# Optimization experiments

Measured on AMD Instinct MI355X. Metric: run time of the kernel, lower is better.

Reference implementation:

```python
import jax, jax.numpy as jnp
import numpy as np

HIDDEN = 2048
NUM_HEADS = 16
Q_LORA = 1536
KV_LORA = 512
QK_NOPE = 128
QK_ROPE = 64
V_HEAD = 128
EPS = 1e-6
QK_HEAD = QK_NOPE + QK_ROPE  # 192


def rmsnorm(x, w, eps=EPS):
    xf = x.astype(jnp.float32)
    var = jnp.mean(xf * xf, axis=-1, keepdims=True)
    return (w * (xf * jax.lax.rsqrt(var + eps)).astype(x.dtype))


def setup_inputs() -> dict:
    key = jax.random.key(0)
    ks = jax.random.split(key, 8)
    B, S = 1, 2048
    hidden_states = jax.random.normal(ks[0], (B, S, HIDDEN), dtype=jnp.float32)
    # causal additive mask [B,1,S,S]
    causal = jnp.tril(jnp.ones((S, S), dtype=bool))
    attention_mask = jnp.where(causal, 0.0, -1e9).astype(jnp.float32)[None, None]
    s = lambda fan_in: 1.0 / np.sqrt(fan_in)
    Wqa = jax.random.normal(ks[1], (HIDDEN, Q_LORA), dtype=jnp.float32) * s(HIDDEN)
    gqa = jnp.ones((Q_LORA,), dtype=jnp.float32)
    Wqb = jax.random.normal(ks[2], (Q_LORA, NUM_HEADS * QK_HEAD), dtype=jnp.float32) * s(Q_LORA)
    Wkva = jax.random.normal(ks[3], (HIDDEN, KV_LORA + QK_ROPE), dtype=jnp.float32) * s(HIDDEN)
    gkva = jnp.ones((KV_LORA,), dtype=jnp.float32)
    Wkvb = jax.random.normal(ks[4], (KV_LORA, NUM_HEADS * (QK_NOPE + V_HEAD)), dtype=jnp.float32) * s(KV_LORA)
    Wo = jax.random.normal(ks[5], (NUM_HEADS * V_HEAD, HIDDEN), dtype=jnp.float32) * s(NUM_HEADS * V_HEAD)
    return {"hidden_states": hidden_states, "attention_mask": attention_mask,
            "Wqa": Wqa, "gqa": gqa, "Wqb": Wqb, "Wkva": Wkva, "gkva": gkva,
            "Wkvb": Wkvb, "Wo": Wo}


def reference(hidden_states, attention_mask, Wqa, gqa, Wqb, Wkva, gkva, Wkvb, Wo):
    B, S, _ = hidden_states.shape
    # Q path: low-rank down-proj + RMSNorm + up-proj
    q_c = rmsnorm(hidden_states @ Wqa, gqa)
    q = (q_c @ Wqb).reshape(B, S, NUM_HEADS, QK_HEAD).transpose(0, 2, 1, 3)  # [B,H,S,192]
    # KV path: joint down-proj, split latent and shared rope part
    kv_c = hidden_states @ Wkva  # [B,S,KV_LORA+ROPE]
    kv_a, k_rope = kv_c[..., :KV_LORA], kv_c[..., KV_LORA:]
    kv = (rmsnorm(kv_a, gkva) @ Wkvb).reshape(B, S, NUM_HEADS, QK_NOPE + V_HEAD)
    k_nope, v = kv[..., :QK_NOPE], kv[..., QK_NOPE:]
    # shared rope part broadcast across heads (no rotary actually applied in source)
    k_rope_b = jnp.broadcast_to(k_rope[:, :, None, :], (B, S, NUM_HEADS, QK_ROPE))
    k = jnp.concatenate([k_nope, k_rope_b], axis=-1).transpose(0, 2, 1, 3)  # [B,H,S,192]
    v = v.transpose(0, 2, 1, 3)  # [B,H,S,128]
    scale = 1.0 / np.sqrt(QK_HEAD)
    attn = jnp.einsum("bhqd,bhkd->bhqk", q, k) * scale
    attn = attn + attention_mask
    attn = jax.nn.softmax(attn.astype(jnp.float32), axis=-1).astype(v.dtype)
    out = jnp.einsum("bhqk,bhkd->bhqd", attn, v)  # [B,H,S,128]
    out = out.transpose(0, 2, 1, 3).reshape(B, S, NUM_HEADS * V_HEAD)
    return out @ Wo
```

## Files before the change

### kernel.cpp

```cpp
#include <hip/hip_runtime.h>
#include <hip/hip_bf16.h>

typedef __bf16 bf16;
typedef __bf16 bf16x8 __attribute__((ext_vector_type(8)));
typedef __bf16 bf16x4 __attribute__((ext_vector_type(4)));
typedef float f32x4 __attribute__((ext_vector_type(4)));

#define HIDDEN 2048
#define SEQ 2048
#define NH 16
#define QL 1536
#define KVL 512
#define SCALE_LOG2E 0.10411754631f

__device__ __forceinline__ void gload_lds16(const void* g, void* l) {
  typedef const __attribute__((address_space(1))) void* gp_t;
  typedef __attribute__((address_space(3))) void* lp_t;
  __builtin_amdgcn_global_load_lds((gp_t)(unsigned long long)g,
                                   (lp_t)(unsigned int)(unsigned long long)l, 16, 0, 0);
}

__device__ __forceinline__ float fexp2(float x) {
  float r; asm("v_exp_f32 %0, %1" : "=v"(r) : "v"(x)); return r;
}

__global__ void k_prep(const float* __restrict__ hidden, bf16* __restrict__ Xb,
                       const float* __restrict__ Wqa, bf16* __restrict__ WqaT,
                       const float* __restrict__ Wqb, bf16* __restrict__ WqbT,
                       const float* __restrict__ Wkva, bf16* __restrict__ WkvaT,
                       const float* __restrict__ Wkvb, bf16* __restrict__ WkvbT,
                       const float* __restrict__ Wo, bf16* __restrict__ WoT) {
  __shared__ float tile[32][33];
  int b = blockIdx.x, tid = threadIdx.x;
  const float* W; bf16* Wt; int K, N, bx, by;
  if (b < 3072)       { W = Wqa;  Wt = WqaT;  K = 2048; N = 1536; int r = b;         bx = r % 48;  by = r / 48; }
  else if (b < 7680)  { W = Wqb;  Wt = WqbT;  K = 1536; N = 3072; int r = b - 3072;  bx = r % 96;  by = r / 96; }
  else if (b < 8832)  { W = Wkva; Wt = WkvaT; K = 2048; N = 576;  int r = b - 7680;  bx = r % 18;  by = r / 18; }
  else if (b < 10880) { W = Wkvb; Wt = WkvbT; K = 512;  N = 4096; int r = b - 8832;  bx = r % 128; by = r / 128; }
  else if (b < 14976) { W = Wo;   Wt = WoT;   K = 2048; N = 2048; int r = b - 10880; bx = r % 64;  by = r / 64; }
  else {
    int r = b - 14976;
    int base = (r * 256 + tid) * 4;
    float4 v = *(const float4*)(hidden + base);
    bf16x4 o = { (bf16)v.x, (bf16)v.y, (bf16)v.z, (bf16)v.w };
    *(bf16x4*)(Xb + base) = o;
    return;
  }
  int n0 = bx * 32, k0 = by * 32, cc = tid & 31, rr = tid >> 5;
#pragma unroll
  for (int it = 0; it < 4; ++it) {
    int r = it * 8 + rr;
    tile[r][cc] = W[(size_t)(k0 + r) * N + n0 + cc];
  }
  __syncthreads();
#pragma unroll
  for (int it = 0; it < 4; ++it) {
    int r = it * 8 + rr;
    Wt[(size_t)(n0 + r) * K + k0 + cc] = (bf16)tile[cc][r];
  }
}

__device__ __forceinline__ void gemm_body(const bf16* __restrict__ A, const bf16* __restrict__ Bt,
                                          bf16* __restrict__ Cb, float* __restrict__ Cf,
                                          int N, int K, int m0, int n0, bf16* As, bf16* Bs) {
  int tid = threadIdx.x, lane = tid & 63, w = tid >> 6;
  int wr = w >> 1, wc = w & 1;
  int l15 = lane & 15, l4 = lane >> 4;
  f32x4 acc[4][4] = {};
  for (int k0 = 0; k0 < K; k0 += 64) {
#pragma unroll
    for (int i = 0; i < 4; ++i) {
      int c = w * 4 + i;
      int row = c * 8 + (lane >> 3);
      int col = (lane & 7) * 8;
      gload_lds16(&A[(size_t)(m0 + row) * K + k0 + col], &As[c * 512]);
      gload_lds16(&Bt[(size_t)(n0 + row) * K + k0 + col], &Bs[c * 512]);
    }
    __syncthreads();
#pragma unroll
    for (int kk = 0; kk < 2; ++kk) {
      bf16x8 af[4], bfr[4];
#pragma unroll
      for (int m = 0; m < 4; ++m)
        af[m] = *(const bf16x8*)&As[(wr * 64 + m * 16 + l15) * 64 + kk * 32 + l4 * 8];
#pragma unroll
      for (int n = 0; n < 4; ++n)
        bfr[n] = *(const bf16x8*)&Bs[(wc * 64 + n * 16 + l15) * 64 + kk * 32 + l4 * 8];
      __builtin_amdgcn_s_setprio(1);
#pragma unroll
      for (int m = 0; m < 4; ++m)
#pragma unroll
        for (int n = 0; n < 4; ++n)
          acc[m][n] = __builtin_amdgcn_mfma_f32_16x16x32_bf16(af[m], bfr[n], acc[m][n], 0, 0, 0);
      __builtin_amdgcn_s_setprio(0);
    }
    __syncthreads();
  }
#pragma unroll
  for (int m = 0; m < 4; ++m)
#pragma unroll
    for (int n = 0; n < 4; ++n)
#pragma unroll
      for (int r = 0; r < 4; ++r) {
        int grow = m0 + wr * 64 + m * 16 + l4 * 4 + r;
        int gcol = n0 + wc * 64 + n * 16 + l15;
        if (gcol < N) {
          float v = acc[m][n][r];
          if (Cf) Cf[(size_t)grow * N + gcol] = v;
          else Cb[(size_t)grow * N + gcol] = (bf16)v;
        }
      }
}

__global__ __launch_bounds__(256) void k_gemm(const bf16* __restrict__ A, const bf16* __restrict__ Bt,
                                              bf16* __restrict__ Cb, float* __restrict__ Cf,
                                              int N, int K) {
  __shared__ __align__(16) bf16 As[128 * 64];
  __shared__ __align__(16) bf16 Bs[128 * 64];
  gemm_body(A, Bt, Cb, Cf, N, K, blockIdx.x * 128, blockIdx.y * 128, As, Bs);
}

__global__ __launch_bounds__(256) void k_gemm_a(const bf16* __restrict__ Xb,
                                                const bf16* __restrict__ B1, const bf16* __restrict__ B2,
                                                float* __restrict__ C1, float* __restrict__ C2) {
  __shared__ __align__(16) bf16 As[128 * 64];
  __shared__ __align__(16) bf16 Bs[128 * 64];
  int by = blockIdx.y;
  if (by < 12) gemm_body(Xb, B1, nullptr, C1, 1536, 2048, blockIdx.x * 128, by * 128, As, Bs);
  else         gemm_body(Xb, B2, nullptr, C2, 576, 2048, blockIdx.x * 128, (by - 12) * 128, As, Bs);
}

__global__ __launch_bounds__(256) void k_gemm_b(const bf16* __restrict__ A1, const bf16* __restrict__ A2,
                                                const bf16* __restrict__ B1, const bf16* __restrict__ B2,
                                                bf16* __restrict__ C1, bf16* __restrict__ C2) {
  __shared__ __align__(16) bf16 As[128 * 64];
  __shared__ __align__(16) bf16 Bs[128 * 64];
  int by = blockIdx.y;
  if (by < 24) gemm_body(A1, B1, C1, nullptr, 3072, 1536, blockIdx.x * 128, by * 128, As, Bs);
  else         gemm_body(A2, B2, C2, nullptr, 4096, 512, blockIdx.x * 128, (by - 24) * 128, As, Bs);
}

__device__ inline float block_reduce_sum(float v, float* red) {
#pragma unroll
  for (int off = 1; off < 64; off <<= 1) v += __shfl_xor(v, off);
  int w = threadIdx.x >> 6;
  if ((threadIdx.x & 63) == 0) red[w] = v;
  __syncthreads();
  return red[0] + red[1] + red[2] + red[3];
}

__global__ void k_rms_all(const float* __restrict__ qa, const float* __restrict__ gq, bf16* __restrict__ qc,
                          const float* __restrict__ kvc, const float* __restrict__ gkv,
                          bf16* __restrict__ kvn, bf16* __restrict__ kr) {
  __shared__ float red[4];
  int b = blockIdx.x, tid = threadIdx.x;
  if (b < 2048) {
    int row = b;
    float v[6];
    float ss = 0.f;
#pragma unroll
    for (int j = 0; j < 6; ++j) {
      v[j] = qa[(size_t)row * QL + tid + j * 256];
      ss += v[j] * v[j];
    }
    float tot = block_reduce_sum(ss, red);
    float rs = rsqrtf(tot / (float)QL + 1e-6f);
#pragma unroll
    for (int j = 0; j < 6; ++j) {
      int c = tid + j * 256;
      qc[(size_t)row * QL + c] = (bf16)(v[j] * rs * gq[c]);
    }
  } else {
    int row = b - 2048;
    float v0 = kvc[(size_t)row * 576 + tid];
    float v1 = kvc[(size_t)row * 576 + tid + 256];
    float tot = block_reduce_sum(v0 * v0 + v1 * v1, red);
    float rs = rsqrtf(tot / (float)KVL + 1e-6f);
    kvn[(size_t)row * KVL + tid] = (bf16)(v0 * rs * gkv[tid]);
    kvn[(size_t)row * KVL + tid + 256] = (bf16)(v1 * rs * gkv[tid + 256]);
    if (tid < 64) kr[row * 64 + tid] = (bf16)kvc[(size_t)row * 576 + 512 + tid];
  }
}

__global__ void k_vt(const bf16* __restrict__ KVm, bf16* __restrict__ VT) {
  __shared__ bf16 tile[32][34];
  int b = blockIdx.x, tid = threadIdx.x;
  int h = b >> 8, rem = b & 255;
  int d0 = (rem >> 6) * 32, s0 = (rem & 63) * 32;
  int cc = tid & 31, rr = tid >> 5;
#pragma unroll
  for (int it = 0; it < 4; ++it) {
    int r = it * 8 + rr;
    tile[r][cc] = KVm[(size_t)(s0 + r) * 4096 + h * 256 + 128 + d0 + cc];
  }
  __syncthreads();
#pragma unroll
  for (int it = 0; it < 4; ++it) {
    int r = it * 8 + rr;
    VT[((size_t)(h * 128 + d0 + r)) * 2048 + s0 + cc] = tile[cc][r];
  }
}

__global__ __launch_bounds__(256) void k_attn(const bf16* __restrict__ Q, const bf16* __restrict__ KV,
                                              const bf16* __restrict__ KR, const bf16* __restrict__ VT,
                                              bf16* __restrict__ O) {
  __shared__ __align__(16) bf16 Ks[64 * 200];
  __shared__ __align__(16) bf16 Vt[128 * 72];
  __shared__ __align__(16) bf16 Ps[4 * 16 * 72];
  int bid = blockIdx.x;
  int h = bid & 15, i = bid >> 4;
  int qb = (i < 16) ? i : 47 - i;
  int q0 = qb * 64;
  int tid = threadIdx.x, lane = tid & 63, w = tid >> 6;
  int l15 = lane & 15, l4 = lane >> 4;
  bf16* Pw = Ps + w * 16 * 72;
  const bf16* VTh = VT + (size_t)h * 128 * 2048;

  bf16x8 aq[6];
  int qrow = q0 + w * 16 + l15;
#pragma unroll
  for (int ks = 0; ks < 6; ++ks)
    aq[ks] = *(const bf16x8*)&Q[(size_t)qrow * 3072 + h * 192 + ks * 32 + l4 * 8];

  bf16x8 ones_b;
  {
    float ov = (l15 == 0) ? 1.0f : 0.0f;
#pragma unroll
    for (int j = 0; j < 8; ++j) ones_b[j] = (bf16)ov;
  }

  f32x4 oacc[8] = {};
  f32x4 o9 = {0.f, 0.f, 0.f, 0.f};
  float m[4] = {-1e30f, -1e30f, -1e30f, -1e30f};
  int nt = qb + 1;
  for (int t = 0; t < nt; ++t) {
#pragma unroll
    for (int it = 0; it < 6; ++it) {
      int idx = it * 256 + tid;
      int r = idx / 24, gg = idx % 24;
      int p = t * 64 + r;
      int4 val;
      if (gg < 16) val = *(const int4*)&KV[(size_t)p * 4096 + h * 256 + gg * 8];
      else         val = *(const int4*)&KR[(size_t)p * 64 + (gg - 16) * 8];
      *(int4*)&Ks[r * 200 + gg * 8] = val;
    }
#pragma unroll
    for (int it = 0; it < 4; ++it) {
      int idx = it * 256 + tid;
      int d = idx >> 3, c = idx & 7;
      *(int4*)&Vt[d * 72 + c * 8] = *(const int4*)&VTh[(size_t)d * 2048 + t * 64 + c * 8];
    }
    __syncthreads();

    f32x4 sacc[4] = {};
    __builtin_amdgcn_s_setprio(1);
#pragma unroll
    for (int ks = 0; ks < 6; ++ks)
#pragma unroll
      for (int n = 0; n < 4; ++n) {
        bf16x8 bk = *(const bf16x8*)&Ks[(n * 16 + l15) * 200 + ks * 32 + l4 * 8];
        sacc[n] = __builtin_amdgcn_mfma_f32_16x16x32_bf16(aq[ks], bk, sacc[n], 0, 0, 0);
      }
    __builtin_amdgcn_s_setprio(0);

    bool lastt = (t == nt - 1);
#pragma unroll
    for (int n = 0; n < 4; ++n)
#pragma unroll
      for (int r = 0; r < 4; ++r) {
        float v = sacc[n][r] * SCALE_LOG2E;
        if (lastt) {
          int col = t * 64 + n * 16 + l15;
          int rowg = q0 + w * 16 + l4 * 4 + r;
          if (col > rowg) v = -1e30f;
        }
        sacc[n][r] = v;
      }

    float pmax[4];
#pragma unroll
    for (int r = 0; r < 4; ++r) {
      float mx = fmaxf(fmaxf(sacc[0][r], sacc[1][r]), fmaxf(sacc[2][r], sacc[3][r]));
      mx = fmaxf(mx, __shfl_xor(mx, 1));
      mx = fmaxf(mx, __shfl_xor(mx, 2));
      mx = fmaxf(mx, __shfl_xor(mx, 4));
      mx = fmaxf(mx, __shfl_xor(mx, 8));
      pmax[r] = mx;
    }
    float need = 0.f;
#pragma unroll
    for (int r = 0; r < 4; ++r) need = fmaxf(need, pmax[r] - m[r]);
    if (__any(need > 8.0f)) {
#pragma unroll
      for (int r = 0; r < 4; ++r) {
        float mn = fmaxf(m[r], pmax[r]);
        float al = fexp2(m[r] - mn);
        m[r] = mn;
#pragma unroll
        for (int vf = 0; vf < 8; ++vf) oacc[vf][r] *= al;
        o9[r] *= al;
      }
    }

#pragma unroll
    for (int n = 0; n < 4; ++n)
#pragma unroll
      for (int r = 0; r < 4; ++r)
        Pw[(l4 * 4 + r) * 72 + n * 16 + l15] = (bf16)fexp2(sacc[n][r] - m[r]);

    __builtin_amdgcn_s_setprio(1);
#pragma unroll
    for (int ks = 0; ks < 2; ++ks) {
      bf16x8 ap = *(const bf16x8*)&Pw[l15 * 72 + ks * 32 + l4 * 8];
      o9 = __builtin_amdgcn_mfma_f32_16x16x32_bf16(ap, ones_b, o9, 0, 0, 0);
#pragma unroll
      for (int vf = 0; vf < 8; ++vf) {
        bf16x8 bv = *(const bf16x8*)&Vt[(vf * 16 + l15) * 72 + ks * 32 + l4 * 8];
        oacc[vf] = __builtin_amdgcn_mfma_f32_16x16x32_bf16(ap, bv, oacc[vf], 0, 0, 0);
      }
    }
    __builtin_amdgcn_s_setprio(0);
    __syncthreads();
  }

#pragma unroll
  for (int r = 0; r < 4; ++r) {
    float ls = __shfl(o9[r], lane & 48);
    float inv = 1.0f / ls;
#pragma unroll
    for (int vf = 0; vf < 8; ++vf) {
      int rowg = q0 + w * 16 + l4 * 4 + r;
      int col = h * 128 + vf * 16 + l15;
      O[(size_t)rowg * 2048 + col] = (bf16)(oacc[vf][r] * inv);
    }
  }
}

extern "C" void kernel_launch(void* const* d_in, const int* in_sizes, int n_in,
                              void* d_out, int out_size, void* d_ws, size_t ws_size,
                              hipStream_t stream) {
  (void)in_sizes; (void)n_in; (void)out_size; (void)ws_size;
  const float* hidden = (const float*)d_in[0];
  const float* Wqa  = (const float*)d_in[2];
  const float* gqa  = (const float*)d_in[3];
  const float* Wqb  = (const float*)d_in[4];
  const float* Wkva = (const float*)d_in[5];
  const float* gkva = (const float*)d_in[6];
  const float* Wkvb = (const float*)d_in[7];
  const float* Wo   = (const float*)d_in[8];
  float* out = (float*)d_out;

  char* ws = (char*)d_ws;
  size_t off = 0;
  auto alloc = [&](size_t bytes) {
    char* p = ws + off;
    off += (bytes + 255) & ~(size_t)255;
    return p;
  };
  bf16* Xb     = (bf16*)alloc((size_t)SEQ * HIDDEN * 2);
  bf16* WqaT   = (bf16*)alloc((size_t)QL * HIDDEN * 2);
  bf16* WqbT   = (bf16*)alloc((size_t)3072 * QL * 2);
  bf16* WkvaT  = (bf16*)alloc((size_t)576 * HIDDEN * 2);
  bf16* WkvbT  = (bf16*)alloc((size_t)4096 * KVL * 2);
  bf16* WoT    = (bf16*)alloc((size_t)2048 * 2048 * 2);
  float* qa    = (float*)alloc((size_t)SEQ * QL * 4);
  float* kvc   = (float*)alloc((size_t)SEQ * 576 * 4);
  bf16* qc     = (bf16*)alloc((size_t)SEQ * QL * 2);
  bf16* kvn    = (bf16*)alloc((size_t)SEQ * KVL * 2);
  bf16* krope  = (bf16*)alloc((size_t)SEQ * 64 * 2);
  bf16* Qm     = (bf16*)alloc((size_t)SEQ * 3072 * 2);
  bf16* KVm    = (bf16*)alloc((size_t)SEQ * 4096 * 2);
  bf16* VTg    = (bf16*)alloc((size_t)NH * 128 * SEQ * 2);
  bf16* Om     = (bf16*)alloc((size_t)SEQ * 2048 * 2);

  k_prep<<<19072, 256, 0, stream>>>(hidden, Xb, Wqa, WqaT, Wqb, WqbT,
                                    Wkva, WkvaT, Wkvb, WkvbT, Wo, WoT);
  k_gemm_a<<<dim3(16, 17), 256, 0, stream>>>(Xb, WqaT, WkvaT, qa, kvc);
  k_rms_all<<<4096, 256, 0, stream>>>(qa, gqa, qc, kvc, gkva, kvn, krope);
  k_gemm_b<<<dim3(16, 56), 256, 0, stream>>>(qc, kvn, WqbT, WkvbT, Qm, KVm);
  k_vt<<<4096, 256, 0, stream>>>(KVm, VTg);
  k_attn<<<512, 256, 0, stream>>>(Qm, KVm, krope, VTg, Om);
  k_gemm<<<dim3(16, 16), 256, 0, stream>>>(Om, WoT, nullptr, out, 2048, 2048);
}
```

Baseline: 244.6 us.

## Split causal attention KV range into chunks with separate combine kernel

Splits each query block's KV loop into chunks of up to 8 tiles (flash-decoding style), raising the grid from 512 to 1280 blocks. Blocks covering more than one chunk write unnormalized bf16 partial outputs plus (max, sum) pairs, and a new combine kernel merges them with log-sum-exp weights. The aim is better load balance and CU occupancy for the long causal rows. The cost is an extra launch, extra partial-output traffic, and bf16 rounding of the unnormalized partials. Partial outputs reuse the qa scratch buffer, which is dead by then.

```diff
diff --git a/kernel.cpp b/kernel.cpp
--- a/kernel.cpp
+++ b/kernel.cpp
@@ -203,13 +203,20 @@
 
 __global__ __launch_bounds__(256) void k_attn(const bf16* __restrict__ Q, const bf16* __restrict__ KV,
                                               const bf16* __restrict__ KR, const bf16* __restrict__ VT,
-                                              bf16* __restrict__ O) {
+                                              bf16* __restrict__ O,
+                                              bf16* __restrict__ Opart, float2* __restrict__ Ml) {
   __shared__ __align__(16) bf16 Ks[64 * 200];
   __shared__ __align__(16) bf16 Vt[128 * 72];
   __shared__ __align__(16) bf16 Ps[4 * 16 * 72];
   int bid = blockIdx.x;
-  int h = bid & 15, i = bid >> 4;
-  int qb = (i < 16) ? i : 47 - i;
+  int h = bid & 15, cid = bid >> 4;
+  int qb, ch, nc;
+  if (cid < 8)       { qb = cid; ch = 0; nc = 1; }
+  else if (cid < 24) { int r = cid - 8;  qb = 8 + (r >> 1); ch = r & 1; nc = 2; }
+  else if (cid < 48) { int r = cid - 24; qb = 16 + r / 3;   ch = r % 3; nc = 3; }
+  else               { int r = cid - 48; qb = 24 + (r >> 2); ch = r & 3; nc = 4; }
+  int t0 = ch * 8;
+  int t1 = t0 + 8 < qb + 1 ? t0 + 8 : qb + 1;
   int q0 = qb * 64;
   int tid = threadIdx.x, lane = tid & 63, w = tid >> 6;
   int l15 = lane & 15, l4 = lane >> 4;
@@ -232,8 +239,7 @@
   f32x4 oacc[8] = {};
   f32x4 o9 = {0.f, 0.f, 0.f, 0.f};
   float m[4] = {-1e30f, -1e30f, -1e30f, -1e30f};
-  int nt = qb + 1;
-  for (int t = 0; t < nt; ++t) {
+  for (int t = t0; t < t1; ++t) {
 #pragma unroll
     for (int it = 0; it < 6; ++it) {
       int idx = it * 256 + tid;
@@ -263,7 +269,7 @@
       }
     __builtin_amdgcn_s_setprio(0);
 
-    bool lastt = (t == nt - 1);
+    bool lastt = (t == qb);
 #pragma unroll
     for (int n = 0; n < 4; ++n)
 #pragma unroll
@@ -323,16 +329,62 @@
     __syncthreads();
   }
 
-#pragma unroll
-  for (int r = 0; r < 4; ++r) {
-    float ls = __shfl(o9[r], lane & 48);
-    float inv = 1.0f / ls;
-#pragma unroll
-    for (int vf = 0; vf < 8; ++vf) {
-      int rowg = q0 + w * 16 + l4 * 4 + r;
-      int col = h * 128 + vf * 16 + l15;
-      O[(size_t)rowg * 2048 + col] = (bf16)(oacc[vf][r] * inv);
-    }
+  if (nc == 1) {
+#pragma unroll
+    for (int r = 0; r < 4; ++r) {
+      float ls = __shfl(o9[r], lane & 48);
+      float inv = 1.0f / ls;
+#pragma unroll
+      for (int vf = 0; vf < 8; ++vf) {
+        int rowg = q0 + w * 16 + l4 * 4 + r;
+        int col = h * 128 + vf * 16 + l15;
+        O[(size_t)rowg * 2048 + col] = (bf16)(oacc[vf][r] * inv);
+      }
+    }
+  } else {
+    bf16* Op = Opart + (size_t)bid * 64 * 128;
+#pragma unroll
+    for (int r = 0; r < 4; ++r) {
+      int row = w * 16 + l4 * 4 + r;
+#pragma unroll
+      for (int vf = 0; vf < 8; ++vf)
+        Op[row * 128 + vf * 16 + l15] = (bf16)oacc[vf][r];
+      if (l15 == 0) Ml[bid * 64 + row] = make_float2(m[r], o9[r]);
+    }
+  }
+}
+
+__global__ __launch_bounds__(256) void k_comb(const bf16* __restrict__ Opart,
+                                              const float2* __restrict__ Ml,
+                                              bf16* __restrict__ O) {
+  int b = blockIdx.x, h = b & 15, qb = 8 + (b >> 4);
+  int cid0, nc;
+  if (qb < 16)      { cid0 = 8 + 2 * (qb - 8);   nc = 2; }
+  else if (qb < 24) { cid0 = 24 + 3 * (qb - 16); nc = 3; }
+  else              { cid0 = 48 + 4 * (qb - 24); nc = 4; }
+  int tid = threadIdx.x;
+  int rr = tid >> 5, col = (tid & 31) * 4;
+  int slot0 = cid0 * 16 + h;
+#pragma unroll
+  for (int rp = 0; rp < 8; ++rp) {
+    int row = rp * 8 + rr;
+    float M = -1e30f;
+    for (int c = 0; c < nc; ++c) M = fmaxf(M, Ml[(slot0 + c * 16) * 64 + row].x);
+    float acc0 = 0.f, acc1 = 0.f, acc2 = 0.f, acc3 = 0.f, L = 0.f;
+    for (int c = 0; c < nc; ++c) {
+      int slot = slot0 + c * 16;
+      float2 ml = Ml[slot * 64 + row];
+      float wgt = fexp2(ml.x - M);
+      L += wgt * ml.y;
+      bf16x4 v = *(const bf16x4*)&Opart[(size_t)slot * 64 * 128 + row * 128 + col];
+      acc0 += wgt * (float)v[0];
+      acc1 += wgt * (float)v[1];
+      acc2 += wgt * (float)v[2];
+      acc3 += wgt * (float)v[3];
+    }
+    float inv = 1.0f / L;
+    bf16x4 o = { (bf16)(acc0 * inv), (bf16)(acc1 * inv), (bf16)(acc2 * inv), (bf16)(acc3 * inv) };
+    *(bf16x4*)&O[(size_t)(qb * 64 + row) * 2048 + h * 128 + col] = o;
   }
 }
 
@@ -372,6 +424,8 @@
   bf16* KVm    = (bf16*)alloc((size_t)SEQ * 4096 * 2);
   bf16* VTg    = (bf16*)alloc((size_t)NH * 128 * SEQ * 2);
   bf16* Om     = (bf16*)alloc((size_t)SEQ * 2048 * 2);
+  float2* Ml   = (float2*)alloc((size_t)1280 * 64 * 8);
+  bf16* Opart  = (bf16*)qa;
 
   k_prep<<<19072, 256, 0, stream>>>(hidden, Xb, Wqa, WqaT, Wqb, WqbT,
                                     Wkva, WkvaT, Wkvb, WkvbT, Wo, WoT);
@@ -379,6 +433,7 @@
   k_rms_all<<<4096, 256, 0, stream>>>(qa, gqa, qc, kvc, gkva, kvn, krope);
   k_gemm_b<<<dim3(16, 56), 256, 0, stream>>>(qc, kvn, WqbT, WkvbT, Qm, KVm);
   k_vt<<<4096, 256, 0, stream>>>(KVm, VTg);
-  k_attn<<<512, 256, 0, stream>>>(Qm, KVm, krope, VTg, Om);
+  k_attn<<<1280, 256, 0, stream>>>(Qm, KVm, krope, VTg, Om, Opart, Ml);
+  k_comb<<<384, 256, 0, stream>>>(Opart, Ml, Om);
   k_gemm<<<dim3(16, 16), 256, 0, stream>>>(Om, WoT, nullptr, out, 2048, 2048);
 }
```

Result: slower. 252.8 us (+3.3%).

## Swizzle attention LDS tiles, use direct global-to-LDS loads and transposed MFMA

Applied to the files above, without the earlier changes.

Rewrites the attention kernel's inner loop. K and V tiles are now loaded with global_load_lds into XOR-swizzled, unpadded LDS layouts instead of going through registers into padded arrays. The MFMA operands are swapped so each lane holds one query column, which lets the row max and row sum be computed with two cross-lane shuffles and a scalar running state. That removes the extra ones-vector MFMA used for the row sum. P is packed with v_cvt_pk_bf16, and the output goes through a swizzled LDS transpose so it can be written with 16-byte stores. The aim is fewer VGPR round-trips, less shuffle and sum overhead, and better-coalesced writes, at the cost of more complex swizzle address arithmetic.

```diff
diff --git a/kernel.cpp b/kernel.cpp
--- a/kernel.cpp
+++ b/kernel.cpp
@@ -22,6 +22,9 @@
 
 __device__ __forceinline__ float fexp2(float x) {
   float r; asm("v_exp_f32 %0, %1" : "=v"(r) : "v"(x)); return r;
+}
+__device__ __forceinline__ unsigned cvt_pk_bf16(float lo, float hi) {
+  unsigned r; asm("v_cvt_pk_bf16_f32 %0, %1, %2" : "=v"(r) : "v"(lo), "v"(hi)); return r;
 }
 
 __global__ void k_prep(const float* __restrict__ hidden, bf16* __restrict__ Xb,
@@ -204,16 +207,17 @@
 __global__ __launch_bounds__(256) void k_attn(const bf16* __restrict__ Q, const bf16* __restrict__ KV,
                                               const bf16* __restrict__ KR, const bf16* __restrict__ VT,
                                               bf16* __restrict__ O) {
-  __shared__ __align__(16) bf16 Ks[64 * 200];
-  __shared__ __align__(16) bf16 Vt[128 * 72];
-  __shared__ __align__(16) bf16 Ps[4 * 16 * 72];
+  __shared__ __align__(16) bf16 Ks[64 * 192];
+  __shared__ __align__(16) bf16 Vt[128 * 64];
+  __shared__ __align__(16) bf16 Ps[4 * 16 * 64];
   int bid = blockIdx.x;
   int h = bid & 15, i = bid >> 4;
   int qb = (i < 16) ? i : 47 - i;
   int q0 = qb * 64;
   int tid = threadIdx.x, lane = tid & 63, w = tid >> 6;
   int l15 = lane & 15, l4 = lane >> 4;
-  bf16* Pw = Ps + w * 16 * 72;
+  int sw = (l15 & 7) << 4;
+  char* PTw = (char*)Ps + w * 2048;
   const bf16* VTh = VT + (size_t)h * 128 * 2048;
 
   bf16x8 aq[6];
@@ -222,117 +226,117 @@
   for (int ks = 0; ks < 6; ++ks)
     aq[ks] = *(const bf16x8*)&Q[(size_t)qrow * 3072 + h * 192 + ks * 32 + l4 * 8];
 
-  bf16x8 ones_b;
-  {
-    float ov = (l15 == 0) ? 1.0f : 0.0f;
-#pragma unroll
-    for (int j = 0; j < 8; ++j) ones_b[j] = (bf16)ov;
-  }
-
   f32x4 oacc[8] = {};
-  f32x4 o9 = {0.f, 0.f, 0.f, 0.f};
-  float m[4] = {-1e30f, -1e30f, -1e30f, -1e30f};
+  float mrun = -1e30f, lrun = 0.f;
   int nt = qb + 1;
   for (int t = 0; t < nt; ++t) {
 #pragma unroll
     for (int it = 0; it < 6; ++it) {
       int idx = it * 256 + tid;
-      int r = idx / 24, gg = idx % 24;
-      int p = t * 64 + r;
-      int4 val;
-      if (gg < 16) val = *(const int4*)&KV[(size_t)p * 4096 + h * 256 + gg * 8];
-      else         val = *(const int4*)&KR[(size_t)p * 64 + (gg - 16) * 8];
-      *(int4*)&Ks[r * 200 + gg * 8] = val;
+      int r = idx / 24, gg = idx - r * 24;
+      int c = gg ^ (r & 7);
+      const bf16* src = (c < 16) ? &KV[(size_t)(t * 64 + r) * 4096 + h * 256 + c * 8]
+                                 : &KR[(size_t)(t * 64 + r) * 64 + (c - 16) * 8];
+      gload_lds16(src, (char*)Ks + (it * 256 + w * 64) * 16);
     }
 #pragma unroll
     for (int it = 0; it < 4; ++it) {
       int idx = it * 256 + tid;
-      int d = idx >> 3, c = idx & 7;
-      *(int4*)&Vt[d * 72 + c * 8] = *(const int4*)&VTh[(size_t)d * 2048 + t * 64 + c * 8];
+      int d = idx >> 3, cc = idx & 7, c = cc ^ (d & 7);
+      gload_lds16(&VTh[(size_t)d * 2048 + t * 64 + c * 8], (char*)Vt + (it * 256 + w * 64) * 16);
     }
     __syncthreads();
 
     f32x4 sacc[4] = {};
     __builtin_amdgcn_s_setprio(1);
 #pragma unroll
-    for (int ks = 0; ks < 6; ++ks)
+    for (int ks = 0; ks < 6; ++ks) {
+      int co = (((ks << 2) + l4) << 4) ^ sw;
 #pragma unroll
       for (int n = 0; n < 4; ++n) {
-        bf16x8 bk = *(const bf16x8*)&Ks[(n * 16 + l15) * 200 + ks * 32 + l4 * 8];
-        sacc[n] = __builtin_amdgcn_mfma_f32_16x16x32_bf16(aq[ks], bk, sacc[n], 0, 0, 0);
+        bf16x8 ak = *(const bf16x8*)((char*)Ks + (n * 16 + l15) * 384 + co);
+        sacc[n] = __builtin_amdgcn_mfma_f32_16x16x32_bf16(ak, aq[ks], sacc[n], 0, 0, 0);
       }
+    }
     __builtin_amdgcn_s_setprio(0);
 
-    bool lastt = (t == nt - 1);
+    bool maskt = (t == qb);
 #pragma unroll
     for (int n = 0; n < 4; ++n)
 #pragma unroll
       for (int r = 0; r < 4; ++r) {
         float v = sacc[n][r] * SCALE_LOG2E;
-        if (lastt) {
-          int col = t * 64 + n * 16 + l15;
-          int rowg = q0 + w * 16 + l4 * 4 + r;
-          if (col > rowg) v = -1e30f;
+        if (maskt) {
+          int kvp = t * 64 + n * 16 + l4 * 4 + r;
+          if (kvp > qrow) v = -1e30f;
         }
         sacc[n][r] = v;
       }
 
-    float pmax[4];
-#pragma unroll
-    for (int r = 0; r < 4; ++r) {
-      float mx = fmaxf(fmaxf(sacc[0][r], sacc[1][r]), fmaxf(sacc[2][r], sacc[3][r]));
-      mx = fmaxf(mx, __shfl_xor(mx, 1));
-      mx = fmaxf(mx, __shfl_xor(mx, 2));
-      mx = fmaxf(mx, __shfl_xor(mx, 4));
-      mx = fmaxf(mx, __shfl_xor(mx, 8));
-      pmax[r] = mx;
-    }
-    float need = 0.f;
-#pragma unroll
-    for (int r = 0; r < 4; ++r) need = fmaxf(need, pmax[r] - m[r]);
-    if (__any(need > 8.0f)) {
-#pragma unroll
-      for (int r = 0; r < 4; ++r) {
-        float mn = fmaxf(m[r], pmax[r]);
-        float al = fexp2(m[r] - mn);
-        m[r] = mn;
-#pragma unroll
-        for (int vf = 0; vf < 8; ++vf) oacc[vf][r] *= al;
-        o9[r] *= al;
-      }
-    }
-
+    float mx = sacc[0][0];
 #pragma unroll
     for (int n = 0; n < 4; ++n)
 #pragma unroll
-      for (int r = 0; r < 4; ++r)
-        Pw[(l4 * 4 + r) * 72 + n * 16 + l15] = (bf16)fexp2(sacc[n][r] - m[r]);
+      for (int r = 0; r < 4; ++r) mx = fmaxf(mx, sacc[n][r]);
+    mx = fmaxf(mx, __shfl_xor(mx, 16));
+    mx = fmaxf(mx, __shfl_xor(mx, 32));
+    if (__any(mx - mrun > 8.0f)) {
+      float mn = fmaxf(mrun, mx);
+      float al = fexp2(mrun - mn);
+      mrun = mn;
+      lrun *= al;
+#pragma unroll
+      for (int vf = 0; vf < 8; ++vf) oacc[vf] *= al;
+    }
+    float rsum = 0.f;
+#pragma unroll
+    for (int n = 0; n < 4; ++n) {
+      float e0 = fexp2(sacc[n][0] - mrun);
+      float e1 = fexp2(sacc[n][1] - mrun);
+      float e2 = fexp2(sacc[n][2] - mrun);
+      float e3 = fexp2(sacc[n][3] - mrun);
+      rsum += (e0 + e1) + (e2 + e3);
+      uint2 u;
+      u.x = cvt_pk_bf16(e0, e1);
+      u.y = cvt_pk_bf16(e2, e3);
+      *(uint2*)(PTw + l15 * 128 + ((n * 32 + l4 * 8) ^ sw)) = u;
+    }
+    rsum += __shfl_xor(rsum, 16);
+    rsum += __shfl_xor(rsum, 32);
+    lrun += rsum;
 
     __builtin_amdgcn_s_setprio(1);
 #pragma unroll
     for (int ks = 0; ks < 2; ++ks) {
-      bf16x8 ap = *(const bf16x8*)&Pw[l15 * 72 + ks * 32 + l4 * 8];
-      o9 = __builtin_amdgcn_mfma_f32_16x16x32_bf16(ap, ones_b, o9, 0, 0, 0);
+      int co = (((ks << 2) + l4) << 4) ^ sw;
+      bf16x8 ap = *(const bf16x8*)(PTw + l15 * 128 + co);
 #pragma unroll
       for (int vf = 0; vf < 8; ++vf) {
-        bf16x8 bv = *(const bf16x8*)&Vt[(vf * 16 + l15) * 72 + ks * 32 + l4 * 8];
-        oacc[vf] = __builtin_amdgcn_mfma_f32_16x16x32_bf16(ap, bv, oacc[vf], 0, 0, 0);
+        bf16x8 av = *(const bf16x8*)((char*)Vt + (vf * 16 + l15) * 128 + co);
+        oacc[vf] = __builtin_amdgcn_mfma_f32_16x16x32_bf16(av, ap, oacc[vf], 0, 0, 0);
       }
     }
     __builtin_amdgcn_s_setprio(0);
     __syncthreads();
   }
 
-#pragma unroll
-  for (int r = 0; r < 4; ++r) {
-    float ls = __shfl(o9[r], lane & 48);
-    float inv = 1.0f / ls;
-#pragma unroll
-    for (int vf = 0; vf < 8; ++vf) {
-      int rowg = q0 + w * 16 + l4 * 4 + r;
-      int col = h * 128 + vf * 16 + l15;
-      O[(size_t)rowg * 2048 + col] = (bf16)(oacc[vf][r] * inv);
-    }
+  char* OTw = (char*)Ks + w * 4096;
+  float inv = 1.0f / lrun;
+#pragma unroll
+  for (int vf = 0; vf < 8; ++vf) {
+    unsigned ua = cvt_pk_bf16(oacc[vf][0] * inv, oacc[vf][1] * inv);
+    unsigned ub = cvt_pk_bf16(oacc[vf][2] * inv, oacc[vf][3] * inv);
+    int base = vf * 32 + l4 * 8;
+    *(unsigned*)(OTw + l15 * 256 + ((base + 0) ^ sw)) = ua;
+    *(unsigned*)(OTw + l15 * 256 + ((base + 4) ^ sw)) = ub;
+  }
+  int qq = lane >> 2, c0 = lane & 3;
+  size_t obase = (size_t)(q0 + w * 16 + qq) * 2048 + h * 128;
+#pragma unroll
+  for (int ii = 0; ii < 4; ++ii) {
+    int ck = ii * 4 + c0;
+    bf16x8 v = *(const bf16x8*)(OTw + qq * 256 + ((ck * 16) ^ ((qq & 7) << 4)));
+    *(bf16x8*)&O[obase + ck * 8] = v;
   }
 }
 
```

After: 236.5 us. 3.3% less time.
